# Kernel tuning notes

Measured on AMD Instinct MI355X. Metric: run time of the kernel, lower is better.

Reference implementation:

```python
import jax, jax.numpy as jnp
import numpy as np

# neuralef_loss_cfg constants (kernel = '10nnn_sigm1.0')
T = 10.0        # cfg['t']
ALPHA = 0.05    # cfg['alpha']
KNN = 10        # parsed from '10nnn'
SIGMA2 = 1.0    # parsed from 'sigm1.0'
EPS = 1e-12     # F.normalize eps

N_TOKENS, D_FEAT, K_EIG = 8192, 768, 256


def setup_inputs() -> dict:
    key = jax.random.key(0)
    k1, k2 = jax.random.split(key)
    FF = jax.random.normal(k1, (N_TOKENS, D_FEAT), dtype=jnp.float32)
    Psi = jax.random.normal(k2, (N_TOKENS, K_EIG), dtype=jnp.float32)
    return {"FF": FF, "Psi": Psi}


def _gram_knn(FF):
    """torch.no_grad() block: RBF affinity -> topk KNN sparsify -> sym -> degree norm."""
    # input_l2_normalize: F.normalize(FF, dim=1)
    FFn = FF / jnp.maximum(jnp.linalg.norm(FF, axis=1, keepdims=True), EPS)
    sq = jnp.sum(FFn * FFn, axis=-1)                       # [N]
    # pairwise squared distances -> RBF kernel  [N, N]
    A = jnp.exp(-(sq[:, None] + sq[None, :] - 2.0 * (FFn @ FFn.T)) / (2.0 * SIGMA2))
    vals, idx = jax.lax.top_k(A, KNN)                      # [N, KNN]
    N = A.shape[0]
    rows = jnp.arange(N)
    # res.scatter_(1, idx, vals) on zeros_like(A)
    res = jnp.zeros_like(A).at[rows[:, None], idx].set(vals)
    gram = 0.5 * (res + res.T)
    gram = gram.at[rows, rows].set(0.0)                    # zero diagonal
    Dsum = jnp.sum(gram, axis=-1)
    # D = Dsum.rsqrt(); D[D==inf] = 0  (Dsum >= 0 always since vals >= 0)
    D = jnp.where(Dsum > 0, jax.lax.rsqrt(Dsum), 0.0)
    return D[:, None] * gram * D[None, :]


def reference(FF, Psi):
    N = Psi.shape[0]
    Psi = Psi * (T / N)
    gram = jax.lax.stop_gradient(_gram_knn(FF))            # [N, N]
    gPsi = gram @ Psi                                      # [N, K]
    R = Psi.T @ gPsi                                       # [K, K]
    # no_sg = False: R_hat = Psi.T.detach() @ gram @ Psi
    R_hat = jax.lax.stop_gradient(Psi).T @ gPsi
    loss = -jnp.trace(R)
    reg = jnp.sum(jnp.triu(R_hat ** 2, 1))
    return jnp.stack([loss, reg * ALPHA])
```

## Files before the change

kernel.cpp:

```cpp
#include <hip/hip_runtime.h>
#include <math.h>

#define N_TOK 8192
#define D_FEAT 768
#define K_EIG 256
#define KNN 10
#define CAP 256
#define NCHUNK 4
#define CHUNK 2048

typedef unsigned short ushort_t;
typedef float f32x4 __attribute__((ext_vector_type(4)));
typedef short bf16x8 __attribute__((ext_vector_type(8)));
typedef unsigned short u16x8 __attribute__((ext_vector_type(8)));
typedef unsigned short u16x4 __attribute__((ext_vector_type(4)));

__device__ inline float u2f(unsigned u) { union { unsigned u; float f; } c; c.u = u; return c.f; }
__device__ inline unsigned f2u(float f) { union { unsigned u; float f; } c; c.f = f; return c.u; }
__device__ inline ushort_t f2bf_rne(float f) {
  const unsigned u = f2u(f);
  return (ushort_t)((u + 0x7fffu + ((u >> 16) & 1u)) >> 16);
}
__device__ inline ushort_t f2key(float f) {
  const unsigned h = f2u(f) >> 16;
  return (ushort_t)((h & 0x8000u) ? (h ^ 0xFFFFu) : (h | 0x8000u));
}
__device__ inline float key2f(unsigned k) {
  const unsigned h = (k & 0x8000u) ? (k ^ 0x8000u) : (k ^ 0xFFFFu);
  return u2f(h << 16);
}
__device__ inline unsigned wave_max_u32(unsigned m) {
#pragma unroll
  for (int s = 1; s < 64; s <<= 1) m = max(m, (unsigned)__shfl_xor((int)m, s, 64));
  return m;
}

__global__ __launch_bounds__(192) void k_norm(const float* __restrict__ FF,
                                              ushort_t* __restrict__ FFbf,
                                              float* __restrict__ rn,
                                              float* __restrict__ sqv) {
  const int row = blockIdx.x;
  const int tid = threadIdx.x;
  const float4 v = *(const float4*)&FF[(size_t)row * D_FEAT + tid * 4];
  float s = v.x * v.x + v.y * v.y + v.z * v.z + v.w * v.w;
  __shared__ float red[3];
  for (int m = 32; m > 0; m >>= 1) s += __shfl_xor(s, m, 64);
  if ((tid & 63) == 0) red[tid >> 6] = s;
  __syncthreads();
  const float tot = red[0] + red[1] + red[2];
  const float scale = 1.f / fmaxf(sqrtf(tot), 1e-12f);
  float4 w;
  w.x = v.x * scale; w.y = v.y * scale; w.z = v.z * scale; w.w = v.w * scale;
  float s2 = w.x * w.x + w.y * w.y + w.z * w.z + w.w * w.w;
  u16x4 o;
  o[0] = f2bf_rne(w.x); o[1] = f2bf_rne(w.y); o[2] = f2bf_rne(w.z); o[3] = f2bf_rne(w.w);
  *(u16x4*)&FFbf[(size_t)row * D_FEAT + tid * 4] = o;
  for (int m = 32; m > 0; m >>= 1) s2 += __shfl_xor(s2, m, 64);
  __syncthreads();
  if ((tid & 63) == 0) red[tid >> 6] = s2;
  __syncthreads();
  if (tid == 0) { sqv[row] = red[0] + red[1] + red[2]; rn[row] = scale; }
}

#define AS1(p) ((const __attribute__((address_space(1))) void*)(p))
#define AS3(p) ((__attribute__((address_space(3))) void*)(p))

__global__ __launch_bounds__(512) void k_gemm(const ushort_t* __restrict__ FFbf,
                                              ushort_t* __restrict__ Cs,
                                              ushort_t* __restrict__ Gmax,
                                              int cbase) {
  __shared__ ushort_t smem[36864];
  const int tid = threadIdx.x;
  const int swz = ((int)blockIdx.x & 7) * 64 + ((int)blockIdx.x >> 3);
  const int mb = swz >> 4;
  const int nb = swz & 15;
  const int rbase = mb * 256;
  const int cb = cbase + nb * 128;
  const int w = tid >> 6, lane = tid & 63;
  const int wr = w >> 1, wc = w & 1;
  const int fr = lane & 15, kg = lane >> 4;
  const int srow = tid >> 2, skq = tid & 3;

  f32x4 acc[4][4];
#pragma unroll
  for (int m = 0; m < 4; ++m)
#pragma unroll
    for (int n = 0; n < 4; ++n) acc[m][n] = (f32x4){0.f, 0.f, 0.f, 0.f};

#define STAGE(b, kt) do { \
    const ushort_t* ga = FFbf + (size_t)(rbase + srow) * D_FEAT + (kt) * 32 + skq * 8; \
    const ushort_t* gb = FFbf + (size_t)(cb + srow) * D_FEAT + (kt) * 32 + skq * 8; \
    char* ab = (char*)smem + (b) * 16384; \
    char* bb = (char*)smem + 49152 + (b) * 8192; \
    __builtin_amdgcn_global_load_lds(AS1(ga), AS3(ab + tid * 16), 16, 0, 0); \
    __builtin_amdgcn_global_load_lds(AS1(ga + (size_t)128 * D_FEAT), AS3(ab + 8192 + tid * 16), 16, 0, 0); \
    __builtin_amdgcn_global_load_lds(AS1(gb), AS3(bb + tid * 16), 16, 0, 0); \
  } while (0)

#define COMPUTE(b) do { \
    bf16x8 af[4], bfr[4]; \
    _Pragma("unroll") \
    for (int m = 0; m < 4; ++m) \
      af[m] = *(const bf16x8*)&smem[(b) * 8192 + (wr * 64 + m * 16 + fr) * 32 + kg * 8]; \
    _Pragma("unroll") \
    for (int n = 0; n < 4; ++n) \
      bfr[n] = *(const bf16x8*)&smem[24576 + (b) * 4096 + (wc * 64 + n * 16 + fr) * 32 + kg * 8]; \
    __builtin_amdgcn_s_setprio(1); \
    _Pragma("unroll") \
    for (int m = 0; m < 4; ++m) \
      _Pragma("unroll") \
      for (int n = 0; n < 4; ++n) \
        acc[m][n] = __builtin_amdgcn_mfma_f32_16x16x32_bf16(af[m], bfr[n], acc[m][n], 0, 0, 0); \
    __builtin_amdgcn_s_setprio(0); \
  } while (0)

#define KSTEP(bR, bS, kt) do { \
    if ((kt) + 1 < 24) { \
      STAGE(bS, (kt) + 1); \
      asm volatile("s_waitcnt vmcnt(3)" ::: "memory"); \
    } else { \
      asm volatile("s_waitcnt vmcnt(0)" ::: "memory"); \
    } \
    __builtin_amdgcn_s_barrier(); \
    __builtin_amdgcn_sched_barrier(0); \
    COMPUTE(bR); \
  } while (0)

  STAGE(0, 0);
  for (int kb = 0; kb < 24; kb += 3) {
    KSTEP(0, 1, kb);
    KSTEP(1, 2, kb + 1);
    KSTEP(2, 0, kb + 2);
  }
#undef KSTEP
#undef COMPUTE
#undef STAGE

  __syncthreads();
#pragma unroll
  for (int m = 0; m < 4; ++m)
#pragma unroll
    for (int n = 0; n < 4; ++n)
#pragma unroll
      for (int r = 0; r < 4; ++r)
        smem[(wr * 64 + m * 16 + kg * 4 + r) * 128 + wc * 64 + n * 16 + fr] = f2key(acc[m][n][r]);
  __syncthreads();
#pragma unroll
  for (int i = 0; i < 8; ++i) {
    const int off = i * 8192 + tid * 16;
    const int row = off >> 8;
    const int colb = off & 255;
    const u16x8 v = *(const u16x8*)((const char*)smem + off);
    *(u16x8*)((char*)Cs + (size_t)(rbase + row) * (CHUNK * 2) + (size_t)nb * 256 + colb) = v;
  }
  {
    const int r2 = tid >> 1;
    const int half = tid & 1;
    u16x8 gmv;
#pragma unroll
    for (int g = 0; g < 8; ++g) {
      const u16x8 grp = *(const u16x8*)&smem[r2 * 128 + half * 64 + g * 8];
      unsigned mx = 0;
#pragma unroll
      for (int j = 0; j < 8; ++j) mx = max(mx, (unsigned)(ushort_t)grp[j]);
      gmv[g] = (ushort_t)mx;
    }
    *(u16x8*)&Gmax[(size_t)(rbase + r2) * 256 + nb * 16 + half * 8] = gmv;
  }
}

__global__ __launch_bounds__(256) void k_sel(const ushort_t* __restrict__ Cs,
                                             const ushort_t* __restrict__ Gmax,
                                             int chunk,
                                             float* __restrict__ pd, int* __restrict__ pi) {
  const int tid = threadIdx.x;
  const int lane = tid & 63;
  const int row = blockIdx.x * 4 + (tid >> 6);
  const ushort_t* src = Cs + (size_t)row * CHUNK;

  const u16x4 gm = *(const u16x4*)&Gmax[(size_t)row * 256 + lane * 4];
  unsigned cur[4];
#pragma unroll
  for (int k = 0; k < 4; ++k)
    cur[k] = (((unsigned)(ushort_t)gm[k]) << 16) | (unsigned)(lane * 4 + k);
  unsigned keep = 0;
#pragma unroll
  for (int r = 0; r < 16; ++r) {
    unsigned m = max(max(cur[0], cur[1]), max(cur[2], cur[3]));
    m = wave_max_u32(m);
    if (lane == r) keep = m;
    const unsigned gid = m & 0xFFu;
    if (lane == (int)(gid >> 2)) {
      const int sl = (int)(gid & 3u);
#pragma unroll
      for (int k = 0; k < 4; ++k)
        if (k == sl) cur[k] = 0;
    }
  }
  const unsigned gid2 = keep & 0xFFu;
  unsigned E[8];
  if (lane < 16) {
    const u16x8 g = *(const u16x8*)&src[gid2 * 8];
#pragma unroll
    for (int j = 0; j < 8; ++j)
      E[j] = (((unsigned)(ushort_t)g[j]) << 16) | (gid2 * 8 + (unsigned)j);
  } else {
#pragma unroll
    for (int j = 0; j < 8; ++j) E[j] = 0;
  }
  unsigned keep2 = 0;
#pragma unroll
  for (int r = 0; r < 16; ++r) {
    unsigned m = E[0];
#pragma unroll
    for (int j = 1; j < 8; ++j) m = max(m, E[j]);
    m = wave_max_u32(m);
    if (lane == r) keep2 = m;
    const unsigned col = m & 0xFFFFu;
    const bool mine = (lane < 16) && ((col >> 3) == gid2);
    const int sl = (int)(col & 7u);
#pragma unroll
    for (int j = 0; j < 8; ++j)
      if (mine && j == sl) E[j] = 0;
  }
  if (lane < 16) {
    pd[((size_t)row * NCHUNK + chunk) * 16 + lane] = key2f(keep2 >> 16);
    pi[((size_t)row * NCHUNK + chunk) * 16 + lane] = chunk * CHUNK + (int)(keep2 & 0xFFFFu);
  }
}

__global__ __launch_bounds__(256) void k_rescore(const float* __restrict__ FF,
                                                 const float* __restrict__ rn,
                                                 const float* __restrict__ sqv,
                                                 const float* __restrict__ pd,
                                                 const int* __restrict__ pi,
                                                 float* __restrict__ tv, int* __restrict__ tj,
                                                 int* __restrict__ cnt) {
  const int tid = threadIdx.x;
  const int lane = tid & 63;
  const int row = blockIdx.x * 4 + (tid >> 6);
  if (lane == 0) cnt[row] = 0;

  const float pdv = pd[(size_t)row * 64 + lane];
  const int myj = pi[(size_t)row * 64 + lane];
  unsigned cur = (((unsigned)f2key(pdv)) << 16) | (unsigned)lane;
  int selj = 0;
#pragma unroll
  for (int r = 0; r < 16; ++r) {
    const unsigned m = wave_max_u32(cur);
    const int wln = (int)(m & 63u);
    const int jw = __shfl(myj, wln, 64);
    if (lane == r) selj = jw;
    if (lane == wln) cur = 0;
  }

  const float si = rn[row];
  const float sqi = sqv[row];
  const float* fi = FF + (size_t)row * D_FEAT;
  float4 a0 = *(const float4*)&fi[lane * 4];
  float4 a1 = *(const float4*)&fi[256 + lane * 4];
  float4 a2 = *(const float4*)&fi[512 + lane * 4];
  a0.x *= si; a0.y *= si; a0.z *= si; a0.w *= si;
  a1.x *= si; a1.y *= si; a1.z *= si; a1.w *= si;
  a2.x *= si; a2.y *= si; a2.z *= si; a2.w *= si;

  float dsc_l = 0.f, dvl_l = 0.f; int j_l = 0;
#pragma unroll 8
  for (int c = 0; c < 16; ++c) {
    const int j = __shfl(selj, c, 64);
    const float sj = rn[j];
    const float* fj = FF + (size_t)j * D_FEAT;
    const float4 b0 = *(const float4*)&fj[lane * 4];
    const float4 b1 = *(const float4*)&fj[256 + lane * 4];
    const float4 b2 = *(const float4*)&fj[512 + lane * 4];
    float acc = 0.f;
    acc = fmaf(a0.x, b0.x * sj, acc); acc = fmaf(a0.y, b0.y * sj, acc);
    acc = fmaf(a0.z, b0.z * sj, acc); acc = fmaf(a0.w, b0.w * sj, acc);
    acc = fmaf(a1.x, b1.x * sj, acc); acc = fmaf(a1.y, b1.y * sj, acc);
    acc = fmaf(a1.z, b1.z * sj, acc); acc = fmaf(a1.w, b1.w * sj, acc);
    acc = fmaf(a2.x, b2.x * sj, acc); acc = fmaf(a2.y, b2.y * sj, acc);
    acc = fmaf(a2.z, b2.z * sj, acc); acc = fmaf(a2.w, b2.w * sj, acc);
#pragma unroll
    for (int m = 32; m > 0; m >>= 1) acc += __shfl_xor(acc, m, 64);
    if (lane == c) {
      const float sqj = sqv[j];
      j_l = j;
      dsc_l = acc - 0.5f * sqj;
      dvl_l = expf(-0.5f * (sqi + sqj - 2.f * acc));
    }
  }

  unsigned fk = 0;
  if (lane < 16) {
    const unsigned u = f2u(dsc_l);
    fk = u ^ ((u >> 31) ? 0xFFFFFFFFu : 0x80000000u);
  }
#pragma unroll
  for (int s = 0; s < 10; ++s) {
    const unsigned m = wave_max_u32(fk);
    const unsigned long long bal = __ballot(fk == m);
    const int wln = __ffsll((unsigned long long)bal) - 1;
    const float tvv = __shfl(dvl_l, wln, 64);
    const int tjj = __shfl(j_l, wln, 64);
    if (lane == s) {
      tv[(size_t)row * KNN + s] = tvv;
      tj[(size_t)row * KNN + s] = tjj;
    }
    if (lane == wln) fk = 0;
  }
}

__global__ void k_scatter(const float* __restrict__ tv, const int* __restrict__ tj,
                          int* __restrict__ cnt, int* __restrict__ nbrJ,
                          float* __restrict__ nbrW) {
  const int e = blockIdx.x * blockDim.x + threadIdx.x;
  if (e >= N_TOK * KNN) return;
  const int i = e / KNN;
  const int j = tj[e];
  if (j == i) return;
  const float w = 0.5f * tv[e];
  const int p = atomicAdd(&cnt[i], 1);
  if (p < CAP) { nbrJ[(size_t)i * CAP + p] = j; nbrW[(size_t)i * CAP + p] = w; }
  const int q = atomicAdd(&cnt[j], 1);
  if (q < CAP) { nbrJ[(size_t)j * CAP + q] = i; nbrW[(size_t)j * CAP + q] = w; }
}

__global__ void k_degree(const int* __restrict__ cnt, const float* __restrict__ nbrW,
                         float* __restrict__ Dv) {
  const int r = blockIdx.x * 4 + (threadIdx.x >> 6);
  const int lane = threadIdx.x & 63;
  const int c = min(cnt[r], CAP);
  float s = 0.f;
  for (int m = lane; m < c; m += 64) s += nbrW[(size_t)r * CAP + m];
  for (int m = 32; m > 0; m >>= 1) s += __shfl_xor(s, m, 64);
  if (lane == 0) Dv[r] = (s > 0.f) ? rsqrtf(s) : 0.f;
}

__global__ __launch_bounds__(256) void k_gpsi(const float* __restrict__ Psi,
                                              const int* __restrict__ cnt,
                                              const int* __restrict__ nbrJ,
                                              const float* __restrict__ nbrW,
                                              const float* __restrict__ Dv,
                                              float* __restrict__ gP) {
  const int i = blockIdx.x;
  const int tid = threadIdx.x;
  __shared__ int sJ[CAP];
  __shared__ float sW[CAP];
  const int c = min(cnt[i], CAP);
  if (tid < c) {
    const int j = nbrJ[(size_t)i * CAP + tid];
    sJ[tid] = j;
    sW[tid] = nbrW[(size_t)i * CAP + tid] * Dv[j];
  }
  __syncthreads();
  float acc = 0.f;
  for (int m = 0; m < c; ++m) acc += sW[m] * Psi[(size_t)sJ[m] * K_EIG + tid];
  gP[(size_t)i * K_EIG + tid] = acc * Dv[i];
}

__global__ __launch_bounds__(256) void k_Rpart(const float* __restrict__ Psi,
                                               const float* __restrict__ gP,
                                               float* __restrict__ Rp) {
  __shared__ float sP[64][68];
  __shared__ float sG[64][68];
  const int tid = threadIdx.x;
  const int ks = blockIdx.x >> 4;
  const int tile = blockIdx.x & 15;
  const int at = (tile >> 2) * 64;
  const int bt = (tile & 3) * 64;
  const int a4 = (tid & 15) * 4;
  const int b4 = (tid >> 4) * 4;
  const int lr = tid >> 2;

  float acc[4][4];
#pragma unroll
  for (int i = 0; i < 4; ++i)
#pragma unroll
    for (int j = 0; j < 4; ++j) acc[i][j] = 0.f;

  for (int rt = 0; rt < 8; ++rt) {
    const int r0 = ks * 512 + rt * 64;
    __syncthreads();
#pragma unroll
    for (int q = 0; q < 4; ++q) {
      const int seg = (tid & 3) + q * 4;
      *(float4*)&sP[lr][seg * 4] = *(const float4*)&Psi[(size_t)(r0 + lr) * K_EIG + at + seg * 4];
      *(float4*)&sG[lr][seg * 4] = *(const float4*)&gP[(size_t)(r0 + lr) * K_EIG + bt + seg * 4];
    }
    __syncthreads();
#pragma unroll 4
    for (int r = 0; r < 64; ++r) {
      const float4 pa = *(const float4*)&sP[r][a4];
      const float4 pg = *(const float4*)&sG[r][b4];
      acc[0][0] = fmaf(pa.x, pg.x, acc[0][0]); acc[0][1] = fmaf(pa.x, pg.y, acc[0][1]);
      acc[0][2] = fmaf(pa.x, pg.z, acc[0][2]); acc[0][3] = fmaf(pa.x, pg.w, acc[0][3]);
      acc[1][0] = fmaf(pa.y, pg.x, acc[1][0]); acc[1][1] = fmaf(pa.y, pg.y, acc[1][1]);
      acc[1][2] = fmaf(pa.y, pg.z, acc[1][2]); acc[1][3] = fmaf(pa.y, pg.w, acc[1][3]);
      acc[2][0] = fmaf(pa.z, pg.x, acc[2][0]); acc[2][1] = fmaf(pa.z, pg.y, acc[2][1]);
      acc[2][2] = fmaf(pa.z, pg.z, acc[2][2]); acc[2][3] = fmaf(pa.z, pg.w, acc[2][3]);
      acc[3][0] = fmaf(pa.w, pg.x, acc[3][0]); acc[3][1] = fmaf(pa.w, pg.y, acc[3][1]);
      acc[3][2] = fmaf(pa.w, pg.z, acc[3][2]); acc[3][3] = fmaf(pa.w, pg.w, acc[3][3]);
    }
  }
#pragma unroll
  for (int i = 0; i < 4; ++i) {
    float4 o; o.x = acc[i][0]; o.y = acc[i][1]; o.z = acc[i][2]; o.w = acc[i][3];
    *(float4*)&Rp[(size_t)ks * (K_EIG * K_EIG) + (size_t)(at + a4 + i) * K_EIG + bt + b4] = o;
  }
}

__global__ __launch_bounds__(256) void k_Rred(const float* __restrict__ Rp,
                                              double* __restrict__ part) {
  const int tid = threadIdx.x;
  const int e0 = blockIdx.x * 1024 + tid * 4;
  float4 s = {0.f, 0.f, 0.f, 0.f};
  for (int ks = 0; ks < 16; ++ks) {
    const float4 v = *(const float4*)&Rp[(size_t)ks * (K_EIG * K_EIG) + e0];
    s.x += v.x; s.y += v.y; s.z += v.z; s.w += v.w;
  }
  const float sc = (10.f / 8192.f) * (10.f / 8192.f);
  double tl = 0.0, rg = 0.0;
#pragma unroll
  for (int j = 0; j < 4; ++j) {
    const int e = e0 + j;
    const int a = e >> 8, b = e & 255;
    const double v = (double)(((const float*)&s)[j] * sc);
    if (a == b) tl += v;
    else if (b > a) rg += v * v;
  }
  __shared__ double st[256], sr[256];
  st[tid] = tl; sr[tid] = rg;
  __syncthreads();
  for (int w = 128; w > 0; w >>= 1) {
    if (tid < w) { st[tid] += st[tid + w]; sr[tid] += sr[tid + w]; }
    __syncthreads();
  }
  if (tid == 0) { part[blockIdx.x] = st[0]; part[64 + blockIdx.x] = sr[0]; }
}

__global__ void k_final2(const double* __restrict__ part, float* __restrict__ out) {
  const int lane = threadIdx.x;
  double tl = part[lane];
  double rg = part[64 + lane];
  for (int m = 32; m > 0; m >>= 1) {
    tl += __shfl_xor(tl, m, 64);
    rg += __shfl_xor(rg, m, 64);
  }
  if (lane == 0) {
    out[0] = (float)(-tl);
    out[1] = (float)(rg * 0.05);
  }
}

extern "C" void kernel_launch(void* const* d_in, const int* in_sizes, int n_in,
                              void* d_out, int out_size, void* d_ws, size_t ws_size,
                              hipStream_t stream) {
  const float* FF = (const float*)d_in[0];
  const float* Psi = (const float*)d_in[1];
  float* out = (float*)d_out;
  float* ws = (float*)d_ws;

  size_t o = 0;
  ushort_t* FFbf = (ushort_t*)(ws + o); o += (size_t)N_TOK * D_FEAT / 2;
  float* rn  = ws + o; o += N_TOK;
  float* sqv = ws + o; o += N_TOK;
  float* pd  = ws + o; o += (size_t)N_TOK * NCHUNK * 16;
  int*   pi  = (int*)(ws + o); o += (size_t)N_TOK * NCHUNK * 16;
  float* tv  = ws + o; o += (size_t)N_TOK * KNN;
  int*   tj  = (int*)(ws + o); o += (size_t)N_TOK * KNN;
  int*   cnt = (int*)(ws + o); o += N_TOK;
  double* part = (double*)(ws + o); o += 256;
  ushort_t* Gmax = (ushort_t*)(ws + o); o += (size_t)N_TOK * 256 / 2;
  char* X = (char*)(ws + o);
  ushort_t* Cs = (ushort_t*)X;
  int*   nbrJ = (int*)X;
  float* nbrW = (float*)(X + (size_t)N_TOK * CAP * 4);
  float* Dv   = (float*)(X + 2 * (size_t)N_TOK * CAP * 4);
  float* gP   = (float*)(X + 2 * (size_t)N_TOK * CAP * 4 + (size_t)N_TOK * 4);
  float* Rp   = (float*)(X + 25ull * 1024 * 1024);

  k_norm<<<N_TOK, 192, 0, stream>>>(FF, FFbf, rn, sqv);
  for (int c = 0; c < NCHUNK; ++c) {
    k_gemm<<<(N_TOK / 256) * (CHUNK / 128), 512, 0, stream>>>(FFbf, Cs, Gmax, c * CHUNK);
    k_sel<<<N_TOK / 4, 256, 0, stream>>>(Cs, Gmax, c, pd, pi);
  }
  k_rescore<<<N_TOK / 4, 256, 0, stream>>>(FF, rn, sqv, pd, pi, tv, tj, cnt);
  k_scatter<<<(N_TOK * KNN + 255) / 256, 256, 0, stream>>>(tv, tj, cnt, nbrJ, nbrW);
  k_degree<<<N_TOK / 4, 256, 0, stream>>>(cnt, nbrW, Dv);
  k_gpsi<<<N_TOK, 256, 0, stream>>>(Psi, cnt, nbrJ, nbrW, Dv, gP);
  k_Rpart<<<256, 256, 0, stream>>>(Psi, gP, Rp);
  k_Rred<<<64, 256, 0, stream>>>(Rp, part);
  k_final2<<<1, 64, 0, stream>>>(part, out);
}
```

Measured before the change: 351.4 us.

## Split GEMM k-step into staggered MFMA halves and fuse scatter into rescore

The GEMM k-step is rewritten so the B-tile global-to-LDS load is issued after the current LDS fragment reads. The 16 MFMAs are split into two halves separated by a barrier, with the remaining A fragments loaded in between, to overlap memory traffic with matrix work. Separately, the KNN scatter is fused into k_rescore, with the cnt zeroing moved into k_norm. This drops one kernel launch and the tv/tj round trip through global memory. The risks are the extra barrier per k-step and reduced overlap inside each wave.

Result: slower. 363.0 us (+3.3%).

```diff
diff --git a/kernel.cpp b/kernel.cpp
--- a/kernel.cpp
+++ b/kernel.cpp
@@ -38,7 +38,8 @@
 __global__ __launch_bounds__(192) void k_norm(const float* __restrict__ FF,
                                               ushort_t* __restrict__ FFbf,
                                               float* __restrict__ rn,
-                                              float* __restrict__ sqv) {
+                                              float* __restrict__ sqv,
+                                              int* __restrict__ cnt) {
   const int row = blockIdx.x;
   const int tid = threadIdx.x;
   const float4 v = *(const float4*)&FF[(size_t)row * D_FEAT + tid * 4];
@@ -59,7 +60,7 @@
   __syncthreads();
   if ((tid & 63) == 0) red[tid >> 6] = s2;
   __syncthreads();
-  if (tid == 0) { sqv[row] = red[0] + red[1] + red[2]; rn[row] = scale; }
+  if (tid == 0) { sqv[row] = red[0] + red[1] + red[2]; rn[row] = scale; cnt[row] = 0; }
 }
 
 #define AS1(p) ((const __attribute__((address_space(1))) void*)(p))
@@ -87,54 +88,74 @@
 #pragma unroll
     for (int n = 0; n < 4; ++n) acc[m][n] = (f32x4){0.f, 0.f, 0.f, 0.f};
 
-#define STAGE(b, kt) do { \
+#define STAGE_A(b, kt) do { \
     const ushort_t* ga = FFbf + (size_t)(rbase + srow) * D_FEAT + (kt) * 32 + skq * 8; \
-    const ushort_t* gb = FFbf + (size_t)(cb + srow) * D_FEAT + (kt) * 32 + skq * 8; \
     char* ab = (char*)smem + (b) * 16384; \
-    char* bb = (char*)smem + 49152 + (b) * 8192; \
     __builtin_amdgcn_global_load_lds(AS1(ga), AS3(ab + tid * 16), 16, 0, 0); \
     __builtin_amdgcn_global_load_lds(AS1(ga + (size_t)128 * D_FEAT), AS3(ab + 8192 + tid * 16), 16, 0, 0); \
+  } while (0)
+
+#define STAGE_B(b, kt) do { \
+    const ushort_t* gb = FFbf + (size_t)(cb + srow) * D_FEAT + (kt) * 32 + skq * 8; \
+    char* bb = (char*)smem + 49152 + (b) * 8192; \
     __builtin_amdgcn_global_load_lds(AS1(gb), AS3(bb + tid * 16), 16, 0, 0); \
   } while (0)
 
-#define COMPUTE(b) do { \
-    bf16x8 af[4], bfr[4]; \
-    _Pragma("unroll") \
-    for (int m = 0; m < 4; ++m) \
-      af[m] = *(const bf16x8*)&smem[(b) * 8192 + (wr * 64 + m * 16 + fr) * 32 + kg * 8]; \
-    _Pragma("unroll") \
-    for (int n = 0; n < 4; ++n) \
-      bfr[n] = *(const bf16x8*)&smem[24576 + (b) * 4096 + (wc * 64 + n * 16 + fr) * 32 + kg * 8]; \
-    __builtin_amdgcn_s_setprio(1); \
-    _Pragma("unroll") \
-    for (int m = 0; m < 4; ++m) \
-      _Pragma("unroll") \
-      for (int n = 0; n < 4; ++n) \
-        acc[m][n] = __builtin_amdgcn_mfma_f32_16x16x32_bf16(af[m], bfr[n], acc[m][n], 0, 0, 0); \
-    __builtin_amdgcn_s_setprio(0); \
-  } while (0)
-
 #define KSTEP(bR, bS, kt) do { \
     if ((kt) + 1 < 24) { \
-      STAGE(bS, (kt) + 1); \
-      asm volatile("s_waitcnt vmcnt(3)" ::: "memory"); \
+      STAGE_A(bS, (kt) + 1); \
+      asm volatile("s_waitcnt vmcnt(2)" ::: "memory"); \
     } else { \
       asm volatile("s_waitcnt vmcnt(0)" ::: "memory"); \
     } \
     __builtin_amdgcn_s_barrier(); \
     __builtin_amdgcn_sched_barrier(0); \
-    COMPUTE(bR); \
+    bf16x8 af0 = *(const bf16x8*)&smem[(bR) * 8192 + (wr * 64 + 0 * 16 + fr) * 32 + kg * 8]; \
+    bf16x8 af1 = *(const bf16x8*)&smem[(bR) * 8192 + (wr * 64 + 1 * 16 + fr) * 32 + kg * 8]; \
+    bf16x8 bf0 = *(const bf16x8*)&smem[24576 + (bR) * 4096 + (wc * 64 + 0 * 16 + fr) * 32 + kg * 8]; \
+    bf16x8 bf1 = *(const bf16x8*)&smem[24576 + (bR) * 4096 + (wc * 64 + 1 * 16 + fr) * 32 + kg * 8]; \
+    bf16x8 bf2 = *(const bf16x8*)&smem[24576 + (bR) * 4096 + (wc * 64 + 2 * 16 + fr) * 32 + kg * 8]; \
+    bf16x8 bf3 = *(const bf16x8*)&smem[24576 + (bR) * 4096 + (wc * 64 + 3 * 16 + fr) * 32 + kg * 8]; \
+    if ((kt) + 1 < 24) STAGE_B(bS, (kt) + 1); \
+    asm volatile("s_waitcnt lgkmcnt(0)" ::: "memory"); \
+    __builtin_amdgcn_sched_barrier(0); \
+    __builtin_amdgcn_s_setprio(1); \
+    acc[0][0] = __builtin_amdgcn_mfma_f32_16x16x32_bf16(af0, bf0, acc[0][0], 0, 0, 0); \
+    acc[0][1] = __builtin_amdgcn_mfma_f32_16x16x32_bf16(af0, bf1, acc[0][1], 0, 0, 0); \
+    acc[0][2] = __builtin_amdgcn_mfma_f32_16x16x32_bf16(af0, bf2, acc[0][2], 0, 0, 0); \
+    acc[0][3] = __builtin_amdgcn_mfma_f32_16x16x32_bf16(af0, bf3, acc[0][3], 0, 0, 0); \
+    acc[1][0] = __builtin_amdgcn_mfma_f32_16x16x32_bf16(af1, bf0, acc[1][0], 0, 0, 0); \
+    acc[1][1] = __builtin_amdgcn_mfma_f32_16x16x32_bf16(af1, bf1, acc[1][1], 0, 0, 0); \
+    acc[1][2] = __builtin_amdgcn_mfma_f32_16x16x32_bf16(af1, bf2, acc[1][2], 0, 0, 0); \
+    acc[1][3] = __builtin_amdgcn_mfma_f32_16x16x32_bf16(af1, bf3, acc[1][3], 0, 0, 0); \
+    __builtin_amdgcn_s_setprio(0); \
+    __builtin_amdgcn_s_barrier(); \
+    bf16x8 af2 = *(const bf16x8*)&smem[(bR) * 8192 + (wr * 64 + 2 * 16 + fr) * 32 + kg * 8]; \
+    bf16x8 af3 = *(const bf16x8*)&smem[(bR) * 8192 + (wr * 64 + 3 * 16 + fr) * 32 + kg * 8]; \
+    asm volatile("s_waitcnt lgkmcnt(0)" ::: "memory"); \
+    __builtin_amdgcn_sched_barrier(0); \
+    __builtin_amdgcn_s_setprio(1); \
+    acc[2][0] = __builtin_amdgcn_mfma_f32_16x16x32_bf16(af2, bf0, acc[2][0], 0, 0, 0); \
+    acc[2][1] = __builtin_amdgcn_mfma_f32_16x16x32_bf16(af2, bf1, acc[2][1], 0, 0, 0); \
+    acc[2][2] = __builtin_amdgcn_mfma_f32_16x16x32_bf16(af2, bf2, acc[2][2], 0, 0, 0); \
+    acc[2][3] = __builtin_amdgcn_mfma_f32_16x16x32_bf16(af2, bf3, acc[2][3], 0, 0, 0); \
+    acc[3][0] = __builtin_amdgcn_mfma_f32_16x16x32_bf16(af3, bf0, acc[3][0], 0, 0, 0); \
+    acc[3][1] = __builtin_amdgcn_mfma_f32_16x16x32_bf16(af3, bf1, acc[3][1], 0, 0, 0); \
+    acc[3][2] = __builtin_amdgcn_mfma_f32_16x16x32_bf16(af3, bf2, acc[3][2], 0, 0, 0); \
+    acc[3][3] = __builtin_amdgcn_mfma_f32_16x16x32_bf16(af3, bf3, acc[3][3], 0, 0, 0); \
+    __builtin_amdgcn_s_setprio(0); \
   } while (0)
 
-  STAGE(0, 0);
+  STAGE_A(0, 0);
+  STAGE_B(0, 0);
   for (int kb = 0; kb < 24; kb += 3) {
     KSTEP(0, 1, kb);
     KSTEP(1, 2, kb + 1);
     KSTEP(2, 0, kb + 2);
   }
 #undef KSTEP
-#undef COMPUTE
-#undef STAGE
+#undef STAGE_B
+#undef STAGE_A
 
   __syncthreads();
 #pragma unroll
@@ -234,12 +255,12 @@
                                                  const float* __restrict__ sqv,
                                                  const float* __restrict__ pd,
                                                  const int* __restrict__ pi,
-                                                 float* __restrict__ tv, int* __restrict__ tj,
-                                                 int* __restrict__ cnt) {
+                                                 int* __restrict__ cnt,
+                                                 int* __restrict__ nbrJ,
+                                                 float* __restrict__ nbrW) {
   const int tid = threadIdx.x;
   const int lane = tid & 63;
   const int row = blockIdx.x * 4 + (tid >> 6);
-  if (lane == 0) cnt[row] = 0;
 
   const float pdv = pd[(size_t)row * 64 + lane];
   const int myj = pi[(size_t)row * 64 + lane];
@@ -295,6 +316,7 @@
     const unsigned u = f2u(dsc_l);
     fk = u ^ ((u >> 31) ? 0xFFFFFFFFu : 0x80000000u);
   }
+  float myTv = 0.f; int myTj = -1;
 #pragma unroll
   for (int s = 0; s < 10; ++s) {
     const unsigned m = wave_max_u32(fk);
@@ -302,27 +324,17 @@
     const int wln = __ffsll((unsigned long long)bal) - 1;
     const float tvv = __shfl(dvl_l, wln, 64);
     const int tjj = __shfl(j_l, wln, 64);
-    if (lane == s) {
-      tv[(size_t)row * KNN + s] = tvv;
-      tj[(size_t)row * KNN + s] = tjj;
-    }
+    if (lane == s) { myTv = tvv; myTj = tjj; }
     if (lane == wln) fk = 0;
   }
-}
-
-__global__ void k_scatter(const float* __restrict__ tv, const int* __restrict__ tj,
-                          int* __restrict__ cnt, int* __restrict__ nbrJ,
-                          float* __restrict__ nbrW) {
-  const int e = blockIdx.x * blockDim.x + threadIdx.x;
-  if (e >= N_TOK * KNN) return;
-  const int i = e / KNN;
-  const int j = tj[e];
-  if (j == i) return;
-  const float w = 0.5f * tv[e];
-  const int p = atomicAdd(&cnt[i], 1);
-  if (p < CAP) { nbrJ[(size_t)i * CAP + p] = j; nbrW[(size_t)i * CAP + p] = w; }
-  const int q = atomicAdd(&cnt[j], 1);
-  if (q < CAP) { nbrJ[(size_t)j * CAP + q] = i; nbrW[(size_t)j * CAP + q] = w; }
+
+  if (lane < KNN && myTj >= 0 && myTj != row) {
+    const float w = 0.5f * myTv;
+    const int p = atomicAdd(&cnt[row], 1);
+    if (p < CAP) { nbrJ[(size_t)row * CAP + p] = myTj; nbrW[(size_t)row * CAP + p] = w; }
+    const int q = atomicAdd(&cnt[myTj], 1);
+    if (q < CAP) { nbrJ[(size_t)myTj * CAP + q] = row; nbrW[(size_t)myTj * CAP + q] = w; }
+  }
 }
 
 __global__ void k_degree(const int* __restrict__ cnt, const float* __restrict__ nbrW,
@@ -466,8 +478,6 @@
   float* sqv = ws + o; o += N_TOK;
   float* pd  = ws + o; o += (size_t)N_TOK * NCHUNK * 16;
   int*   pi  = (int*)(ws + o); o += (size_t)N_TOK * NCHUNK * 16;
-  float* tv  = ws + o; o += (size_t)N_TOK * KNN;
-  int*   tj  = (int*)(ws + o); o += (size_t)N_TOK * KNN;
   int*   cnt = (int*)(ws + o); o += N_TOK;
   double* part = (double*)(ws + o); o += 256;
   ushort_t* Gmax = (ushort_t*)(ws + o); o += (size_t)N_TOK * 256 / 2;
@@ -479,13 +489,12 @@
   float* gP   = (float*)(X + 2 * (size_t)N_TOK * CAP * 4 + (size_t)N_TOK * 4);
   float* Rp   = (float*)(X + 25ull * 1024 * 1024);
 
-  k_norm<<<N_TOK, 192, 0, stream>>>(FF, FFbf, rn, sqv);
+  k_norm<<<N_TOK, 192, 0, stream>>>(FF, FFbf, rn, sqv, cnt);
   for (int c = 0; c < NCHUNK; ++c) {
     k_gemm<<<(N_TOK / 256) * (CHUNK / 128), 512, 0, stream>>>(FFbf, Cs, Gmax, c * CHUNK);
     k_sel<<<N_TOK / 4, 256, 0, stream>>>(Cs, Gmax, c, pd, pi);
   }
-  k_rescore<<<N_TOK / 4, 256, 0, stream>>>(FF, rn, sqv, pd, pi, tv, tj, cnt);
-  k_scatter<<<(N_TOK * KNN + 255) / 256, 256, 0, stream>>>(tv, tj, cnt, nbrJ, nbrW);
+  k_rescore<<<N_TOK / 4, 256, 0, stream>>>(FF, rn, sqv, pd, pi, cnt, nbrJ, nbrW);
   k_degree<<<N_TOK / 4, 256, 0, stream>>>(cnt, nbrW, Dv);
   k_gpsi<<<N_TOK, 256, 0, stream>>>(Psi, cnt, nbrJ, nbrW, Dv, gP);
   k_Rpart<<<256, 256, 0, stream>>>(Psi, gP, Rp);
```
